# Performance work log

Hardware: AMD Instinct MI355X
Metric: run time of the kernel (lower is better)

Reference implementation:

```python
import jax, jax.numpy as jnp
import numpy as np

N, E, D, L = 100000, 600000, 128, 5
EPS = 1e-5


def setup_inputs() -> dict:
    key = jax.random.key(0)
    ks = jax.random.split(key, 32)
    ri = lambda k, shape, hi: jax.random.randint(k, shape, 0, hi)
    rn = lambda k, shape: jax.random.normal(k, shape, jnp.float32) * 0.02
    inp = {
        'atomic_num': ri(ks[0], (N,), 119),
        'formal_charge': ri(ks[1], (N,), 11),
        'chiral_tag': ri(ks[2], (N,), 5),
        'hybridization': ri(ks[3], (N,), 8),
        'num_explicit_hs': ri(ks[4], (N,), 6),
        'is_aromatic': ri(ks[5], (N,), 2),
        'edge_index': ri(ks[6], (2, E), N),
        'is_conjugated': ri(ks[7], (E,), 2),
        'edge_is_aromatic': ri(ks[8], (E,), 2),
        'bond_type': ri(ks[9], (E,), 22),
        'bond_dir': ri(ks[10], (E,), 7),
        'bond_stereo': ri(ks[11], (E,), 6),
        # atom embedding tables (vocab sizes are typical RDKit cardinalities)
        'emb_atomic_num': rn(ks[12], (120, D)),
        'emb_formal_charge': rn(ks[13], (12, D)),
        'emb_chiral_tag': rn(ks[14], (5, D)),
        'emb_hybridization': rn(ks[15], (8, D)),
        'emb_num_explicit_hs': rn(ks[16], (6, D)),
        'emb_is_aromatic': rn(ks[17], (2, D)),
        # per-layer edge embedding tables, stacked on leading layer axis
        'e_conj': rn(ks[18], (L, 3, D)),
        'e_arom': rn(ks[19], (L, 3, D)),
        'e_btype': rn(ks[20], (L, 23, D)),
        'e_bdir': rn(ks[21], (L, 8, D)),
        'e_bstereo': rn(ks[22], (L, 7, D)),
        # per-layer GIN MLP (D -> 2D -> D)
        'mlp_w1': rn(ks[23], (L, D, 2 * D)),
        'mlp_b1': jnp.zeros((L, 2 * D), jnp.float32),
        'mlp_w2': rn(ks[24], (L, 2 * D, D)),
        'mlp_b2': jnp.zeros((L, D), jnp.float32),
        # per-layer batchnorm affine params (training-mode batch stats)
        'bn_gamma': jnp.ones((L, D), jnp.float32),
        'bn_beta': jnp.zeros((L, D), jnp.float32),
    }
    return inp


def reference(atomic_num, formal_charge, chiral_tag, hybridization,
              num_explicit_hs, is_aromatic, edge_index,
              is_conjugated, edge_is_aromatic, bond_type, bond_dir, bond_stereo,
              emb_atomic_num, emb_formal_charge, emb_chiral_tag,
              emb_hybridization, emb_num_explicit_hs, emb_is_aromatic,
              e_conj, e_arom, e_btype, e_bdir, e_bstereo,
              mlp_w1, mlp_b1, mlp_w2, mlp_b2, bn_gamma, bn_beta):
    # seed node features: sum of atom-feature embeddings  [N, D]
    h = (emb_atomic_num[atomic_num] + emb_formal_charge[formal_charge]
         + emb_chiral_tag[chiral_tag] + emb_hybridization[hybridization]
         + emb_num_explicit_hs[num_explicit_hs] + emb_is_aromatic[is_aromatic])
    src, dst = edge_index[0], edge_index[1]
    for l in range(L):
        # edge embeddings: sum of bond-feature embeddings  [E, D]
        eemb = (e_conj[l][is_conjugated] + e_arom[l][edge_is_aromatic]
                + e_btype[l][bond_type] + e_bdir[l][bond_dir]
                + e_bstereo[l][bond_stereo])
        # self-loop edges use bond-feature index 0 for every feature  [D]
        self_vec = e_conj[l, 0] + e_arom[l, 0] + e_btype[l, 0] + e_bdir[l, 0] + e_bstereo[l, 0]
        # GIN message: x_j + edge_attr, scatter-add at dst; self loops folded in analytically
        msg = h[src] + eemb                                      # [E, D]
        agg = jax.ops.segment_sum(msg, dst, num_segments=N) + h + self_vec
        # GIN update MLP: D -> 2D -> D
        hid = jax.nn.relu(agg @ mlp_w1[l] + mlp_b1[l])
        h = hid @ mlp_w2[l] + mlp_b2[l]
        # batch norm over the node dimension (training-mode batch statistics)
        mean = h.mean(axis=0)
        var = h.var(axis=0)
        h = bn_gamma[l] * (h - mean) * jax.lax.rsqrt(var + EPS) + bn_beta[l]
        if l < L - 1:
            h = jax.nn.relu(h)
        # dropout_ratio = 0.0 -> identity
    return h  # JK='last', graph_pooling=None -> node representations [N, D]
```

## Files before the change

kernel.cpp:

```cpp
#include <hip/hip_runtime.h>

#define NN 100000
#define EE 600000
#define DD 128
#define LL 5
#define CTROWS 5152
#define MBLK 1563
#define TILES 1563
#define PBLK 256
#define SBLK 98

typedef float f32x4 __attribute__((ext_vector_type(4)));
typedef _Float16 f16x8 __attribute__((ext_vector_type(8)));
typedef _Float16 f16x4 __attribute__((ext_vector_type(4)));

__global__ __launch_bounds__(256) void seed_kernel(
    const int* __restrict__ an, const int* __restrict__ fc,
    const int* __restrict__ ct, const int* __restrict__ hy,
    const int* __restrict__ nh, const int* __restrict__ ar,
    const float* __restrict__ ean, const float* __restrict__ efc,
    const float* __restrict__ ect, const float* __restrict__ ehy,
    const float* __restrict__ enh, const float* __restrict__ ear,
    _Float16* __restrict__ h)
{
    int idx = blockIdx.x * 256 + threadIdx.x;
    int n = idx >> 4, q = idx & 15;
    f32x4 a0 = ((const f32x4*)(ean + an[n] * DD))[2 * q];
    f32x4 a1 = ((const f32x4*)(ean + an[n] * DD))[2 * q + 1];
    a0 += ((const f32x4*)(efc + fc[n] * DD))[2 * q];
    a1 += ((const f32x4*)(efc + fc[n] * DD))[2 * q + 1];
    a0 += ((const f32x4*)(ect + ct[n] * DD))[2 * q];
    a1 += ((const f32x4*)(ect + ct[n] * DD))[2 * q + 1];
    a0 += ((const f32x4*)(ehy + hy[n] * DD))[2 * q];
    a1 += ((const f32x4*)(ehy + hy[n] * DD))[2 * q + 1];
    a0 += ((const f32x4*)(enh + nh[n] * DD))[2 * q];
    a1 += ((const f32x4*)(enh + nh[n] * DD))[2 * q + 1];
    a0 += ((const f32x4*)(ear + ar[n] * DD))[2 * q];
    a1 += ((const f32x4*)(ear + ar[n] * DD))[2 * q + 1];
    f16x8 o;
    #pragma unroll
    for (int j = 0; j < 4; ++j) { o[j] = (_Float16)a0[j]; o[j + 4] = (_Float16)a1[j]; }
    ((f16x8*)h)[idx] = o;
}

__global__ __launch_bounds__(256) void convw1_kernel(const float* __restrict__ w1,
                                                     _Float16* __restrict__ w1t)
{
    int idx = blockIdx.x * 256 + threadIdx.x;
    int l = idx >> 15, rem = idx & 32767;
    int n = rem >> 7, k = rem & 127;
    w1t[idx] = (_Float16)w1[l * 32768 + k * 256 + n];
}
__global__ __launch_bounds__(256) void convw2_kernel(const float* __restrict__ w2,
                                                     _Float16* __restrict__ w2t)
{
    int idx = blockIdx.x * 256 + threadIdx.x;
    int l = idx >> 15, rem = idx & 32767;
    int n = rem >> 8, k = rem & 255;
    w2t[idx] = (_Float16)w2[l * 32768 + k * 128 + n];
}

__global__ void idss_kernel(float* __restrict__ idss)
{
    int t = threadIdx.x;
    idss[t] = (t < 128) ? 1.0f : 0.0f;
}

__global__ __launch_bounds__(256) void count_kernel(const int* __restrict__ ei,
                                                    int* __restrict__ cursor)
{
    int e = blockIdx.x * 256 + threadIdx.x;
    if (e < EE) atomicAdd(&cursor[ei[EE + e]], 1);
}

__global__ __launch_bounds__(1024) void btot_kernel(const int* __restrict__ cursor,
                                                    int* __restrict__ btot)
{
    __shared__ int wsum[16];
    int tid = threadIdx.x;
    int i = blockIdx.x * 1024 + tid;
    int x = (i < NN) ? cursor[i] : 0;
    #pragma unroll
    for (int off = 1; off < 64; off <<= 1) x += __shfl_xor(x, off, 64);
    if ((tid & 63) == 0) wsum[tid >> 6] = x;
    __syncthreads();
    if (tid == 0) {
        int s = 0;
        #pragma unroll
        for (int w = 0; w < 16; ++w) s += wsum[w];
        btot[blockIdx.x] = s;
    }
}

__global__ __launch_bounds__(128) void bscan_kernel(const int* __restrict__ btot,
                                                    int* __restrict__ boff,
                                                    int* __restrict__ rowstart)
{
    __shared__ int w0;
    int t = threadIdx.x;
    int lane = t & 63, wv = t >> 6;
    int x = (t < SBLK) ? btot[t] : 0;
    int incl = x;
    #pragma unroll
    for (int off = 1; off < 64; off <<= 1) {
        int u = __shfl_up(incl, off, 64);
        if (lane >= off) incl += u;
    }
    if (wv == 0 && lane == 63) w0 = incl;
    __syncthreads();
    if (wv == 1) incl += w0;
    if (t < SBLK) boff[t] = incl - x;
    if (t == 127) rowstart[NN] = incl;
}

__global__ __launch_bounds__(1024) void apply_kernel(const int* __restrict__ cursorin,
                                                     const int* __restrict__ boff,
                                                     int* __restrict__ rowstart,
                                                     int* __restrict__ cursor)
{
    __shared__ int wsum[16];
    int tid = threadIdx.x;
    int lane = tid & 63, wv = tid >> 6;
    int i = blockIdx.x * 1024 + tid;
    int x = (i < NN) ? cursorin[i] : 0;
    int incl = x;
    #pragma unroll
    for (int off = 1; off < 64; off <<= 1) {
        int u = __shfl_up(incl, off, 64);
        if (lane >= off) incl += u;
    }
    if (lane == 63) wsum[wv] = incl;
    __syncthreads();
    int pre = 0;
    #pragma unroll
    for (int w = 0; w < 16; ++w) pre += (w < wv) ? wsum[w] : 0;
    int excl = boff[blockIdx.x] + pre + incl - x;
    if (i < NN) { rowstart[i] = excl; cursor[i] = excl; }
}

__global__ __launch_bounds__(256) void fill_kernel(
    const int* __restrict__ ei, int* __restrict__ cursor, int* __restrict__ rec,
    const int* __restrict__ f0, const int* __restrict__ f1,
    const int* __restrict__ f2, const int* __restrict__ f3,
    const int* __restrict__ f4)
{
    int e = blockIdx.x * 256 + threadIdx.x;
    if (e >= EE) return;
    int dst = ei[EE + e];
    int p = atomicAdd(&cursor[dst], 1);
    int f = f0[e] + 2 * (f1[e] + 2 * (f2[e] + 23 * (f3[e] + 8 * f4[e])));
    rec[p] = ei[e] | (f << 17);
}

__global__ __launch_bounds__(256) void ctab_kernel(
    const float* __restrict__ ec, const float* __restrict__ ea,
    const float* __restrict__ eb, const float* __restrict__ ed,
    const float* __restrict__ es, _Float16* __restrict__ ctab5)
{
    int idx = blockIdx.x * 256 + threadIdx.x;
    int q = idx & 15;
    int grow = idx >> 4;
    int l = grow / CTROWS, row = grow - l * CTROWS;
    int conj = row & 1, arom = (row >> 1) & 1;
    int r2 = row >> 2;
    int bt = r2 % 23, r3 = r2 / 23;
    int bd = r3 & 7, bs = r3 >> 3;
    const float* ecl = ec + l * 3 * DD;
    const float* eal = ea + l * 3 * DD;
    const float* ebl = eb + l * 23 * DD;
    const float* edl = ed + l * 8 * DD;
    const float* esl = es + l * 7 * DD;
    f32x4 a0 = ((const f32x4*)(ecl + conj * DD))[2 * q]
             + ((const f32x4*)(eal + arom * DD))[2 * q]
             + ((const f32x4*)(ebl + bt * DD))[2 * q]
             + ((const f32x4*)(edl + bd * DD))[2 * q]
             + ((const f32x4*)(esl + bs * DD))[2 * q];
    f32x4 a1 = ((const f32x4*)(ecl + conj * DD))[2 * q + 1]
             + ((const f32x4*)(eal + arom * DD))[2 * q + 1]
             + ((const f32x4*)(ebl + bt * DD))[2 * q + 1]
             + ((const f32x4*)(edl + bd * DD))[2 * q + 1]
             + ((const f32x4*)(esl + bs * DD))[2 * q + 1];
    f16x8 o;
    #pragma unroll
    for (int j = 0; j < 4; ++j) { o[j] = (_Float16)a0[j]; o[j + 4] = (_Float16)a1[j]; }
    ((f16x8*)ctab5)[idx] = o;
}

__global__ __launch_bounds__(256) void gather_bn_kernel(
    const _Float16* __restrict__ hsrc, _Float16* __restrict__ agg,
    const int* __restrict__ rowstart, const int* __restrict__ rec,
    const _Float16* __restrict__ ctab, const float* __restrict__ ss, int dorelu)
{
    int idx = blockIdx.x * 256 + threadIdx.x;
    int n = idx >> 4, q = idx & 15;
    f16x8 sc8, sh8, clampv;
    _Float16 cl = dorelu ? (_Float16)0.0f : (_Float16)(-60000.0f);
    #pragma unroll
    for (int j = 0; j < 8; ++j) {
        sc8[j] = (_Float16)ss[q * 8 + j];
        sh8[j] = (_Float16)ss[128 + q * 8 + j];
        clampv[j] = cl;
    }
    int p0 = rowstart[n], p1 = rowstart[n + 1];
    f16x8 x = ((const f16x8*)hsrc)[idx];
    f16x8 c0 = ((const f16x8*)ctab)[q];
    f16x8 ts = __builtin_elementwise_max((f16x8)(x * sc8 + sh8), clampv);
    float v[8];
    #pragma unroll
    for (int j = 0; j < 8; ++j) v[j] = (float)ts[j] + (float)c0[j];

    if (p0 < p1) {
        int r0 = rec[p0];
        int r1 = (p0 + 1 < p1) ? rec[p0 + 1] : r0;
        int rr2 = (p0 + 2 < p1) ? rec[p0 + 2] : r1;
        f16x8 y0 = *(const f16x8*)(hsrc + (size_t)(r0 & 0x1FFFF) * DD + q * 8);
        f16x8 e0 = *(const f16x8*)(ctab + (size_t)(((unsigned)r0) >> 17) * DD + q * 8);
        f16x8 y1 = *(const f16x8*)(hsrc + (size_t)(r1 & 0x1FFFF) * DD + q * 8);
        f16x8 e1 = *(const f16x8*)(ctab + (size_t)(((unsigned)r1) >> 17) * DD + q * 8);
        for (int p = p0; p < p1; ++p) {
            int r3 = (p + 3 < p1) ? rec[p + 3] : rr2;
            f16x8 y2 = *(const f16x8*)(hsrc + (size_t)(rr2 & 0x1FFFF) * DD + q * 8);
            f16x8 e2 = *(const f16x8*)(ctab + (size_t)(((unsigned)rr2) >> 17) * DD + q * 8);
            f16x8 t = __builtin_elementwise_max((f16x8)(y0 * sc8 + sh8), clampv);
            f16x8 u = t + e0;
            #pragma unroll
            for (int j = 0; j < 8; ++j) v[j] += (float)u[j];
            y0 = y1; e0 = e1; y1 = y2; e1 = e2; rr2 = r3;
        }
    }
    f16x8 o;
    #pragma unroll
    for (int j = 0; j < 8; ++j) o[j] = (_Float16)v[j];
    ((f16x8*)agg)[idx] = o;
}

__global__ __launch_bounds__(256, 1) void mlp_kernel(
    const _Float16* __restrict__ A, const _Float16* __restrict__ w1t,
    const _Float16* __restrict__ w2t,
    const float* __restrict__ b1, const float* __restrict__ b2,
    _Float16* __restrict__ hpre, float* __restrict__ psum, float* __restrict__ psq,
    int M)
{
    __shared__ _Float16 hid[2][8 * 4 * 64 * 8];
    int tid = threadIdx.x;
    int w = tid >> 6, lane = tid & 63;
    int ln = lane & 15, quad = lane >> 4;
    const f32x4 zero = {0.f, 0.f, 0.f, 0.f};

    int t0 = (blockIdx.x * TILES) >> 8;
    int t1 = ((blockIdx.x + 1) * TILES) >> 8;

    f16x8 ba[4][4];
    #pragma unroll
    for (int ns = 0; ns < 4; ++ns) {
        int row = t0 * 64 + ns * 16 + ln;
        row = row < M ? row : M - 1;
        #pragma unroll
        for (int kt = 0; kt < 4; ++kt)
            ba[ns][kt] = *(const f16x8*)(A + (size_t)row * 128 + kt * 32 + quad * 8);
    }

    f16x8 w1f[4][4];
    #pragma unroll
    for (int n1 = 0; n1 < 4; ++n1)
        #pragma unroll
        for (int kt = 0; kt < 4; ++kt)
            w1f[n1][kt] = *(const f16x8*)(w1t + (w * 64 + n1 * 16 + ln) * 128 + kt * 32 + quad * 8);
    f32x4 b1v[4];
    #pragma unroll
    for (int n1 = 0; n1 < 4; ++n1)
        b1v[n1] = *(const f32x4*)(b1 + w * 64 + n1 * 16 + quad * 4);

    f16x8 w2f[2][8];
    #pragma unroll
    for (int n2 = 0; n2 < 2; ++n2)
        #pragma unroll
        for (int kt2 = 0; kt2 < 8; ++kt2)
            w2f[n2][kt2] = *(const f16x8*)(w2t + (w * 32 + n2 * 16 + ln) * 256 + kt2 * 32 + quad * 8);
    f32x4 b2v[2];
    #pragma unroll
    for (int n2 = 0; n2 < 2; ++n2)
        b2v[n2] = *(const f32x4*)(b2 + w * 32 + n2 * 16 + quad * 4);

    f32x4 ssum[2] = {zero, zero};
    f32x4 sqsum[2] = {zero, zero};

    for (int t = t0; t < t1; ++t) {
        int node0 = t * 64;
        _Float16* hb = hid[t & 1];

        #pragma unroll
        for (int ns = 0; ns < 4; ++ns) {
            f32x4 acc1[4] = {zero, zero, zero, zero};
            #pragma unroll
            for (int kt = 0; kt < 4; ++kt)
                #pragma unroll
                for (int n1 = 0; n1 < 4; ++n1)
                    acc1[n1] = __builtin_amdgcn_mfma_f32_16x16x32_f16(w1f[n1][kt], ba[ns][kt], acc1[n1], 0, 0, 0);
            {
                int row = (t + 1) * 64 + ns * 16 + ln;
                row = row < M ? row : M - 1;
                #pragma unroll
                for (int kt = 0; kt < 4; ++kt)
                    ba[ns][kt] = *(const f16x8*)(A + (size_t)row * 128 + kt * 32 + quad * 8);
            }
            #pragma unroll
            for (int n1 = 0; n1 < 4; ++n1) {
                int a = w * 4 + n1;
                f16x4 pk;
                #pragma unroll
                for (int r = 0; r < 4; ++r) {
                    float v = acc1[n1][r] + b1v[n1][r];
                    v = v > 0.f ? v : 0.f;
                    pk[r] = (_Float16)v;
                }
                int lp = ((a & 1) * 2 + (quad >> 1)) * 16 + ln;
                int off = (((a >> 1) * 4 + ns) * 64 + lp) * 8 + (quad & 1) * 4;
                *(f16x4*)(hb + off) = pk;
            }
        }

        __syncthreads();

        #pragma unroll
        for (int ns = 0; ns < 4; ++ns) {
            f32x4 acc2[2] = {zero, zero};
            #pragma unroll
            for (int kt2 = 0; kt2 < 8; ++kt2) {
                f16x8 bf = *(const f16x8*)(hb + ((kt2 * 4 + ns) * 64 + lane) * 8);
                acc2[0] = __builtin_amdgcn_mfma_f32_16x16x32_f16(w2f[0][kt2], bf, acc2[0], 0, 0, 0);
                acc2[1] = __builtin_amdgcn_mfma_f32_16x16x32_f16(w2f[1][kt2], bf, acc2[1], 0, 0, 0);
            }
            int node = node0 + ns * 16 + ln;
            bool valid = node < M;
            #pragma unroll
            for (int n2 = 0; n2 < 2; ++n2) {
                f32x4 v;
                f16x4 pk;
                #pragma unroll
                for (int r = 0; r < 4; ++r) {
                    v[r] = acc2[n2][r] + b2v[n2][r];
                    pk[r] = (_Float16)v[r];
                }
                if (valid) {
                    *(f16x4*)(hpre + (size_t)node * 128 + w * 32 + n2 * 16 + quad * 4) = pk;
                    ssum[n2] += v;
                    sqsum[n2] += v * v;
                }
            }
        }
    }

    #pragma unroll
    for (int n2 = 0; n2 < 2; ++n2)
        #pragma unroll
        for (int off = 1; off < 16; off <<= 1)
            #pragma unroll
            for (int r = 0; r < 4; ++r) {
                ssum[n2][r] += __shfl_xor(ssum[n2][r], off, 64);
                sqsum[n2][r] += __shfl_xor(sqsum[n2][r], off, 64);
            }
    if (ln == 0) {
        #pragma unroll
        for (int n2 = 0; n2 < 2; ++n2) {
            *(f32x4*)(psum + blockIdx.x * 128 + w * 32 + n2 * 16 + quad * 4) = ssum[n2];
            *(f32x4*)(psq + blockIdx.x * 128 + w * 32 + n2 * 16 + quad * 4) = sqsum[n2];
        }
    }
}

__global__ __launch_bounds__(256) void reduce_kernel(
    const float* __restrict__ psum, const float* __restrict__ psq,
    const float* __restrict__ gamma, const float* __restrict__ beta,
    float* __restrict__ ss, int nblk)
{
    int c = blockIdx.x;
    int tid = threadIdx.x;
    float s = 0.f, q = 0.f;
    for (int b = tid; b < nblk; b += 256) {
        s += psum[b * 128 + c];
        q += psq[b * 128 + c];
    }
    #pragma unroll
    for (int off = 1; off < 64; off <<= 1) {
        s += __shfl_xor(s, off, 64);
        q += __shfl_xor(q, off, 64);
    }
    __shared__ float rs[4], rq[4];
    int wave = tid >> 6;
    if ((tid & 63) == 0) { rs[wave] = s; rq[wave] = q; }
    __syncthreads();
    if (tid == 0) {
        s = rs[0] + rs[1] + rs[2] + rs[3];
        q = rq[0] + rq[1] + rq[2] + rq[3];
        const float invN = 1.0f / NN;
        float mean = s * invN;
        float var = q * invN - mean * mean;
        float inv = rsqrtf(var + 1e-5f);
        float scale = gamma[c] * inv;
        ss[c] = scale;
        ss[128 + c] = beta[c] - mean * scale;
    }
}

__global__ __launch_bounds__(256) void final_bn_kernel(
    const _Float16* __restrict__ hpre, float* __restrict__ out,
    const float* __restrict__ ss)
{
    int idx = blockIdx.x * 256 + threadIdx.x;
    int q = idx & 15;
    f16x8 x = ((const f16x8*)hpre)[idx];
    f32x4 sc0 = ((const f32x4*)ss)[2 * q],        sc1 = ((const f32x4*)ss)[2 * q + 1];
    f32x4 sh0 = ((const f32x4*)(ss + 128))[2 * q], sh1 = ((const f32x4*)(ss + 128))[2 * q + 1];
    f32x4 y0, y1;
    #pragma unroll
    for (int j = 0; j < 4; ++j) {
        y0[j] = (float)x[j] * sc0[j] + sh0[j];
        y1[j] = (float)x[j + 4] * sc1[j] + sh1[j];
    }
    ((f32x4*)out)[2 * idx] = y0;
    ((f32x4*)out)[2 * idx + 1] = y1;
}

extern "C" void kernel_launch(void* const* d_in, const int* in_sizes, int n_in,
                              void* d_out, int out_size, void* d_ws, size_t ws_size,
                              hipStream_t stream)
{
    const int* an  = (const int*)d_in[0];
    const int* fc  = (const int*)d_in[1];
    const int* ct  = (const int*)d_in[2];
    const int* hy  = (const int*)d_in[3];
    const int* nh  = (const int*)d_in[4];
    const int* ar  = (const int*)d_in[5];
    const int* ei  = (const int*)d_in[6];
    const int* econ = (const int*)d_in[7];
    const int* earo = (const int*)d_in[8];
    const int* ebt  = (const int*)d_in[9];
    const int* ebd  = (const int*)d_in[10];
    const int* ebs  = (const int*)d_in[11];
    const float* ean = (const float*)d_in[12];
    const float* efc = (const float*)d_in[13];
    const float* ect = (const float*)d_in[14];
    const float* ehy = (const float*)d_in[15];
    const float* enh = (const float*)d_in[16];
    const float* ear = (const float*)d_in[17];
    const float* e_conj   = (const float*)d_in[18];
    const float* e_arom   = (const float*)d_in[19];
    const float* e_btype  = (const float*)d_in[20];
    const float* e_bdir   = (const float*)d_in[21];
    const float* e_bstereo= (const float*)d_in[22];
    const float* mlp_w1 = (const float*)d_in[23];
    const float* mlp_b1 = (const float*)d_in[24];
    const float* mlp_w2 = (const float*)d_in[25];
    const float* mlp_b2 = (const float*)d_in[26];
    const float* bn_gamma = (const float*)d_in[27];
    const float* bn_beta  = (const float*)d_in[28];

    _Float16* h0   = (_Float16*)d_ws;
    _Float16* agg  = h0 + (size_t)NN * DD;
    _Float16* hpre = agg + (size_t)NN * DD;
    _Float16* w1t  = hpre + (size_t)NN * DD;
    _Float16* w2t  = w1t + LL * 256 * 128;
    _Float16* ctab5= w2t + LL * 128 * 256;
    float*    psum = (float*)(ctab5 + (size_t)LL * CTROWS * DD);
    float*    psq  = psum + MBLK * 128;
    float*    ss   = psq + MBLK * 128;
    float*    idss = ss + 256;
    int* rowstart = (int*)(idss + 256);
    int* cursor   = rowstart + NN + 8;
    int* rec      = cursor + NN;
    int* btot     = rec + EE;
    int* boff     = btot + SBLK + 8;

    convw1_kernel<<<640, 256, 0, stream>>>(mlp_w1, w1t);
    convw2_kernel<<<640, 256, 0, stream>>>(mlp_w2, w2t);
    seed_kernel<<<6250, 256, 0, stream>>>(an, fc, ct, hy, nh, ar,
                                          ean, efc, ect, ehy, enh, ear, h0);
    idss_kernel<<<1, 256, 0, stream>>>(idss);
    ctab_kernel<<<1610, 256, 0, stream>>>(e_conj, e_arom, e_btype,
                                          e_bdir, e_bstereo, ctab5);

    hipMemsetAsync(cursor, 0, NN * sizeof(int), stream);
    count_kernel<<<2344, 256, 0, stream>>>(ei, cursor);
    btot_kernel<<<SBLK, 1024, 0, stream>>>(cursor, btot);
    bscan_kernel<<<1, 128, 0, stream>>>(btot, boff, rowstart);
    apply_kernel<<<SBLK, 1024, 0, stream>>>(cursor, boff, rowstart, cursor);
    fill_kernel<<<2344, 256, 0, stream>>>(ei, cursor, rec,
                                          econ, earo, ebt, ebd, ebs);

    for (int l = 0; l < LL; ++l) {
        gather_bn_kernel<<<6250, 256, 0, stream>>>(
            (l == 0) ? h0 : hpre, agg, rowstart, rec,
            ctab5 + (size_t)l * CTROWS * DD,
            (l == 0) ? idss : ss, (l == 0) ? 0 : 1);
        mlp_kernel<<<PBLK, 256, 0, stream>>>(
            agg, w1t + l * 32768, w2t + l * 32768,
            mlp_b1 + l * 256, mlp_b2 + l * 128,
            hpre, psum, psq, NN);
        reduce_kernel<<<128, 256, 0, stream>>>(
            psum, psq, bn_gamma + l * 128, bn_beta + l * 128, ss, PBLK);
    }
    final_bn_kernel<<<6250, 256, 0, stream>>>(hpre, (float*)d_out, ss);
}
```

Measured before the change: 570.9 us.

## Fuse neighbor gather and BN-apply into the per-layer MLP kernel

Merges the per-node gather/aggregate kernel into the MFMA MLP kernel. Each tile's 64 aggregated rows are now built in LDS instead of being written to and re-read from a global agg buffer, and the two node buffers ping-pong between layers. The three small setup kernels (two weight conversions and the identity scale init) are also merged into one launch. The trade-off is that the irregular gather now runs inside only 256 persistent blocks at one block per CU, which gives far less latency hiding than the 6250-block standalone gather. A single LDS hid buffer is used where there used to be two.

```diff
diff --git a/kernel.cpp b/kernel.cpp
--- a/kernel.cpp
+++ b/kernel.cpp
@@ -43,27 +43,26 @@
     ((f16x8*)h)[idx] = o;
 }
 
-__global__ __launch_bounds__(256) void convw1_kernel(const float* __restrict__ w1,
-                                                     _Float16* __restrict__ w1t)
-{
-    int idx = blockIdx.x * 256 + threadIdx.x;
-    int l = idx >> 15, rem = idx & 32767;
-    int n = rem >> 7, k = rem & 127;
-    w1t[idx] = (_Float16)w1[l * 32768 + k * 256 + n];
-}
-__global__ __launch_bounds__(256) void convw2_kernel(const float* __restrict__ w2,
-                                                     _Float16* __restrict__ w2t)
-{
-    int idx = blockIdx.x * 256 + threadIdx.x;
-    int l = idx >> 15, rem = idx & 32767;
-    int n = rem >> 8, k = rem & 255;
-    w2t[idx] = (_Float16)w2[l * 32768 + k * 128 + n];
-}
-
-__global__ void idss_kernel(float* __restrict__ idss)
-{
-    int t = threadIdx.x;
-    idss[t] = (t < 128) ? 1.0f : 0.0f;
+__global__ __launch_bounds__(256) void convw_kernel(
+    const float* __restrict__ w1, const float* __restrict__ w2,
+    _Float16* __restrict__ w1t, _Float16* __restrict__ w2t,
+    float* __restrict__ idss)
+{
+    int b = blockIdx.x;
+    if (b < 640) {
+        int idx = b * 256 + threadIdx.x;
+        int l = idx >> 15, rem = idx & 32767;
+        int n = rem >> 7, k = rem & 127;
+        w1t[idx] = (_Float16)w1[l * 32768 + k * 256 + n];
+    } else if (b < 1280) {
+        int idx = (b - 640) * 256 + threadIdx.x;
+        int l = idx >> 15, rem = idx & 32767;
+        int n = rem >> 8, k = rem & 255;
+        w2t[idx] = (_Float16)w2[l * 32768 + k * 128 + n];
+    } else {
+        int t = threadIdx.x;
+        idss[t] = (t < 128) ? 1.0f : 0.0f;
+    }
 }
 
 __global__ __launch_bounds__(256) void count_kernel(const int* __restrict__ ei,
@@ -186,13 +185,24 @@
     ((f16x8*)ctab5)[idx] = o;
 }
 
-__global__ __launch_bounds__(256) void gather_bn_kernel(
-    const _Float16* __restrict__ hsrc, _Float16* __restrict__ agg,
+__global__ __launch_bounds__(256, 1) void layer_kernel(
+    const _Float16* __restrict__ hsrc, _Float16* __restrict__ hdst,
     const int* __restrict__ rowstart, const int* __restrict__ rec,
-    const _Float16* __restrict__ ctab, const float* __restrict__ ss, int dorelu)
-{
-    int idx = blockIdx.x * 256 + threadIdx.x;
-    int n = idx >> 4, q = idx & 15;
+    const _Float16* __restrict__ ctab, const float* __restrict__ ss,
+    const _Float16* __restrict__ w1t, const _Float16* __restrict__ w2t,
+    const float* __restrict__ b1, const float* __restrict__ b2,
+    float* __restrict__ psum, float* __restrict__ psq,
+    int dorelu, int M)
+{
+    __shared__ _Float16 hid[8 * 4 * 64 * 8];
+    __shared__ _Float16 at[16 * 64 * 8];
+    int tid = threadIdx.x;
+    int w = tid >> 6, lane = tid & 63;
+    int ln = lane & 15, quad = lane >> 4;
+    int u = tid >> 4;
+    int q = tid & 15;
+    const f32x4 zero = {0.f, 0.f, 0.f, 0.f};
+
     f16x8 sc8, sh8, clampv;
     _Float16 cl = dorelu ? (_Float16)0.0f : (_Float16)(-60000.0f);
     #pragma unroll
@@ -201,64 +211,9 @@
         sh8[j] = (_Float16)ss[128 + q * 8 + j];
         clampv[j] = cl;
     }
-    int p0 = rowstart[n], p1 = rowstart[n + 1];
-    f16x8 x = ((const f16x8*)hsrc)[idx];
-    f16x8 c0 = ((const f16x8*)ctab)[q];
-    f16x8 ts = __builtin_elementwise_max((f16x8)(x * sc8 + sh8), clampv);
-    float v[8];
-    #pragma unroll
-    for (int j = 0; j < 8; ++j) v[j] = (float)ts[j] + (float)c0[j];
-
-    if (p0 < p1) {
-        int r0 = rec[p0];
-        int r1 = (p0 + 1 < p1) ? rec[p0 + 1] : r0;
-        int rr2 = (p0 + 2 < p1) ? rec[p0 + 2] : r1;
-        f16x8 y0 = *(const f16x8*)(hsrc + (size_t)(r0 & 0x1FFFF) * DD + q * 8);
-        f16x8 e0 = *(const f16x8*)(ctab + (size_t)(((unsigned)r0) >> 17) * DD + q * 8);
-        f16x8 y1 = *(const f16x8*)(hsrc + (size_t)(r1 & 0x1FFFF) * DD + q * 8);
-        f16x8 e1 = *(const f16x8*)(ctab + (size_t)(((unsigned)r1) >> 17) * DD + q * 8);
-        for (int p = p0; p < p1; ++p) {
-            int r3 = (p + 3 < p1) ? rec[p + 3] : rr2;
-            f16x8 y2 = *(const f16x8*)(hsrc + (size_t)(rr2 & 0x1FFFF) * DD + q * 8);
-            f16x8 e2 = *(const f16x8*)(ctab + (size_t)(((unsigned)rr2) >> 17) * DD + q * 8);
-            f16x8 t = __builtin_elementwise_max((f16x8)(y0 * sc8 + sh8), clampv);
-            f16x8 u = t + e0;
-            #pragma unroll
-            for (int j = 0; j < 8; ++j) v[j] += (float)u[j];
-            y0 = y1; e0 = e1; y1 = y2; e1 = e2; rr2 = r3;
-        }
-    }
-    f16x8 o;
-    #pragma unroll
-    for (int j = 0; j < 8; ++j) o[j] = (_Float16)v[j];
-    ((f16x8*)agg)[idx] = o;
-}
-
-__global__ __launch_bounds__(256, 1) void mlp_kernel(
-    const _Float16* __restrict__ A, const _Float16* __restrict__ w1t,
-    const _Float16* __restrict__ w2t,
-    const float* __restrict__ b1, const float* __restrict__ b2,
-    _Float16* __restrict__ hpre, float* __restrict__ psum, float* __restrict__ psq,
-    int M)
-{
-    __shared__ _Float16 hid[2][8 * 4 * 64 * 8];
-    int tid = threadIdx.x;
-    int w = tid >> 6, lane = tid & 63;
-    int ln = lane & 15, quad = lane >> 4;
-    const f32x4 zero = {0.f, 0.f, 0.f, 0.f};
-
-    int t0 = (blockIdx.x * TILES) >> 8;
-    int t1 = ((blockIdx.x + 1) * TILES) >> 8;
-
-    f16x8 ba[4][4];
-    #pragma unroll
-    for (int ns = 0; ns < 4; ++ns) {
-        int row = t0 * 64 + ns * 16 + ln;
-        row = row < M ? row : M - 1;
-        #pragma unroll
-        for (int kt = 0; kt < 4; ++kt)
-            ba[ns][kt] = *(const f16x8*)(A + (size_t)row * 128 + kt * 32 + quad * 8);
-    }
+    f16x8 c0 = *(const f16x8*)(ctab + q * 8);
+    int ktw = q >> 2, quadw = q & 3;
+    int lanep = quadw * 16 + (u & 15);
 
     f16x8 w1f[4][4];
     #pragma unroll
@@ -270,7 +225,6 @@
     #pragma unroll
     for (int n1 = 0; n1 < 4; ++n1)
         b1v[n1] = *(const f32x4*)(b1 + w * 64 + n1 * 16 + quad * 4);
-
     f16x8 w2f[2][8];
     #pragma unroll
     for (int n2 = 0; n2 < 2; ++n2)
@@ -285,38 +239,84 @@
     f32x4 ssum[2] = {zero, zero};
     f32x4 sqsum[2] = {zero, zero};
 
+    int t0 = (blockIdx.x * TILES) >> 8;
+    int t1 = ((blockIdx.x + 1) * TILES) >> 8;
+
     for (int t = t0; t < t1; ++t) {
         int node0 = t * 64;
-        _Float16* hb = hid[t & 1];
+
+        int pp0[4], pp1[4];
+        f16x8 xv[4];
+        #pragma unroll
+        for (int pass = 0; pass < 4; ++pass) {
+            int n = node0 + pass * 16 + u;
+            int nc = n < M ? n : M - 1;
+            pp0[pass] = rowstart[nc];
+            pp1[pass] = rowstart[nc + 1];
+            xv[pass] = *(const f16x8*)(hsrc + (size_t)nc * 128 + q * 8);
+        }
+        #pragma unroll
+        for (int pass = 0; pass < 4; ++pass) {
+            int p0 = pp0[pass], p1 = pp1[pass];
+            f16x8 ts = __builtin_elementwise_max((f16x8)(xv[pass] * sc8 + sh8), clampv);
+            float v[8];
+            #pragma unroll
+            for (int j = 0; j < 8; ++j) v[j] = (float)ts[j] + (float)c0[j];
+            if (p0 < p1) {
+                int r0 = rec[p0];
+                int r1 = (p0 + 1 < p1) ? rec[p0 + 1] : r0;
+                int rr2 = (p0 + 2 < p1) ? rec[p0 + 2] : r1;
+                f16x8 y0 = *(const f16x8*)(hsrc + (size_t)(r0 & 0x1FFFF) * DD + q * 8);
+                f16x8 e0 = *(const f16x8*)(ctab + (size_t)(((unsigned)r0) >> 17) * DD + q * 8);
+                f16x8 y1 = *(const f16x8*)(hsrc + (size_t)(r1 & 0x1FFFF) * DD + q * 8);
+                f16x8 e1 = *(const f16x8*)(ctab + (size_t)(((unsigned)r1) >> 17) * DD + q * 8);
+                for (int p = p0; p < p1; ++p) {
+                    int r3 = (p + 3 < p1) ? rec[p + 3] : rr2;
+                    f16x8 y2 = *(const f16x8*)(hsrc + (size_t)(rr2 & 0x1FFFF) * DD + q * 8);
+                    f16x8 e2 = *(const f16x8*)(ctab + (size_t)(((unsigned)rr2) >> 17) * DD + q * 8);
+                    f16x8 tt = __builtin_elementwise_max((f16x8)(y0 * sc8 + sh8), clampv);
+                    f16x8 uu = tt + e0;
+                    #pragma unroll
+                    for (int j = 0; j < 8; ++j) v[j] += (float)uu[j];
+                    y0 = y1; e0 = e1; y1 = y2; e1 = e2; rr2 = r3;
+                }
+            }
+            f16x8 o;
+            #pragma unroll
+            for (int j = 0; j < 8; ++j) o[j] = (_Float16)v[j];
+            int F = ktw * 4 + pass;
+            *(f16x8*)(at + (F * 64 + (lanep ^ (F & 7))) * 8) = o;
+        }
+
+        __syncthreads();
 
         #pragma unroll
         for (int ns = 0; ns < 4; ++ns) {
+            f16x8 bak[4];
+            #pragma unroll
+            for (int kt = 0; kt < 4; ++kt) {
+                int F = kt * 4 + ns;
+                bak[kt] = *(const f16x8*)(at + (F * 64 + (lane ^ (F & 7))) * 8);
+            }
             f32x4 acc1[4] = {zero, zero, zero, zero};
             #pragma unroll
             for (int kt = 0; kt < 4; ++kt)
                 #pragma unroll
                 for (int n1 = 0; n1 < 4; ++n1)
-                    acc1[n1] = __builtin_amdgcn_mfma_f32_16x16x32_f16(w1f[n1][kt], ba[ns][kt], acc1[n1], 0, 0, 0);
-            {
-                int row = (t + 1) * 64 + ns * 16 + ln;
-                row = row < M ? row : M - 1;
-                #pragma unroll
-                for (int kt = 0; kt < 4; ++kt)
-                    ba[ns][kt] = *(const f16x8*)(A + (size_t)row * 128 + kt * 32 + quad * 8);
-            }
+                    acc1[n1] = __builtin_amdgcn_mfma_f32_16x16x32_f16(w1f[n1][kt], bak[kt], acc1[n1], 0, 0, 0);
             #pragma unroll
             for (int n1 = 0; n1 < 4; ++n1) {
                 int a = w * 4 + n1;
                 f16x4 pk;
                 #pragma unroll
                 for (int r = 0; r < 4; ++r) {
-                    float v = acc1[n1][r] + b1v[n1][r];
-                    v = v > 0.f ? v : 0.f;
-                    pk[r] = (_Float16)v;
+                    float vv = acc1[n1][r] + b1v[n1][r];
+                    vv = vv > 0.f ? vv : 0.f;
+                    pk[r] = (_Float16)vv;
                 }
                 int lp = ((a & 1) * 2 + (quad >> 1)) * 16 + ln;
                 int off = (((a >> 1) * 4 + ns) * 64 + lp) * 8 + (quad & 1) * 4;
-                *(f16x4*)(hb + off) = pk;
+                *(f16x4*)(hid + off) = pk;
             }
         }
 
@@ -327,7 +327,7 @@
             f32x4 acc2[2] = {zero, zero};
             #pragma unroll
             for (int kt2 = 0; kt2 < 8; ++kt2) {
-                f16x8 bf = *(const f16x8*)(hb + ((kt2 * 4 + ns) * 64 + lane) * 8);
+                f16x8 bf = *(const f16x8*)(hid + ((kt2 * 4 + ns) * 64 + lane) * 8);
                 acc2[0] = __builtin_amdgcn_mfma_f32_16x16x32_f16(w2f[0][kt2], bf, acc2[0], 0, 0, 0);
                 acc2[1] = __builtin_amdgcn_mfma_f32_16x16x32_f16(w2f[1][kt2], bf, acc2[1], 0, 0, 0);
             }
@@ -335,17 +335,17 @@
             bool valid = node < M;
             #pragma unroll
             for (int n2 = 0; n2 < 2; ++n2) {
-                f32x4 v;
+                f32x4 vv;
                 f16x4 pk;
                 #pragma unroll
                 for (int r = 0; r < 4; ++r) {
-                    v[r] = acc2[n2][r] + b2v[n2][r];
-                    pk[r] = (_Float16)v[r];
+                    vv[r] = acc2[n2][r] + b2v[n2][r];
+                    pk[r] = (_Float16)vv[r];
                 }
                 if (valid) {
-                    *(f16x4*)(hpre + (size_t)node * 128 + w * 32 + n2 * 16 + quad * 4) = pk;
-                    ssum[n2] += v;
-                    sqsum[n2] += v * v;
+                    *(f16x4*)(hdst + (size_t)node * 128 + w * 32 + n2 * 16 + quad * 4) = pk;
+                    ssum[n2] += vv;
+                    sqsum[n2] += vv * vv;
                 }
             }
         }
@@ -457,8 +457,7 @@
     const float* bn_beta  = (const float*)d_in[28];
 
     _Float16* h0   = (_Float16*)d_ws;
-    _Float16* agg  = h0 + (size_t)NN * DD;
-    _Float16* hpre = agg + (size_t)NN * DD;
+    _Float16* hpre = h0 + (size_t)NN * DD;
     _Float16* w1t  = hpre + (size_t)NN * DD;
     _Float16* w2t  = w1t + LL * 256 * 128;
     _Float16* ctab5= w2t + LL * 128 * 256;
@@ -472,11 +471,9 @@
     int* btot     = rec + EE;
     int* boff     = btot + SBLK + 8;
 
-    convw1_kernel<<<640, 256, 0, stream>>>(mlp_w1, w1t);
-    convw2_kernel<<<640, 256, 0, stream>>>(mlp_w2, w2t);
+    convw_kernel<<<1281, 256, 0, stream>>>(mlp_w1, mlp_w2, w1t, w2t, idss);
     seed_kernel<<<6250, 256, 0, stream>>>(an, fc, ct, hy, nh, ar,
                                           ean, efc, ect, ehy, enh, ear, h0);
-    idss_kernel<<<1, 256, 0, stream>>>(idss);
     ctab_kernel<<<1610, 256, 0, stream>>>(e_conj, e_arom, e_btype,
                                           e_bdir, e_bstereo, ctab5);
 
@@ -489,14 +486,15 @@
                                           econ, earo, ebt, ebd, ebs);
 
     for (int l = 0; l < LL; ++l) {
-        gather_bn_kernel<<<6250, 256, 0, stream>>>(
-            (l == 0) ? h0 : hpre, agg, rowstart, rec,
+        const _Float16* src = (l & 1) ? hpre : h0;
+        _Float16* dst = (l & 1) ? h0 : hpre;
+        layer_kernel<<<PBLK, 256, 0, stream>>>(
+            src, dst, rowstart, rec,
             ctab5 + (size_t)l * CTROWS * DD,
-            (l == 0) ? idss : ss, (l == 0) ? 0 : 1);
-        mlp_kernel<<<PBLK, 256, 0, stream>>>(
-            agg, w1t + l * 32768, w2t + l * 32768,
+            (l == 0) ? idss : ss,
+            w1t + l * 32768, w2t + l * 32768,
             mlp_b1 + l * 256, mlp_b2 + l * 128,
-            hpre, psum, psq, NN);
+            psum, psq, (l == 0) ? 0 : 1, NN);
         reduce_kernel<<<128, 256, 0, stream>>>(
             psum, psq, bn_gamma + l * 128, bn_beta + l * 128, ss, PBLK);
     }
```

New measurement: 951.8 us. 1.67x slower.
